# Kernel tuning notes

Measured on AMD Instinct MI355X. Metric: run time of the kernel, lower is better.

Reference implementation:

```python
import jax, jax.numpy as jnp
import numpy as np

N_NODES, N_EDGES, IN_FEATS, N_HIDDEN, K_HOP = 100000, 400000, 128, 128, 3


def setup_inputs() -> dict:
    key = jax.random.key(0)
    ks = jax.random.split(key, 12)
    x = jax.random.normal(ks[0], (N_NODES, IN_FEATS), jnp.float32)
    src = jax.random.randint(ks[1], (N_EDGES,), 0, N_NODES, jnp.int32)
    dst = jax.random.randint(ks[2], (N_EDGES,), 0, N_NODES, jnp.int32)
    neg_src = jax.random.randint(ks[3], (N_EDGES,), 0, N_NODES, jnp.int32)
    neg_dst = jax.random.randint(ks[4], (N_EDGES,), 0, N_NODES, jnp.int32)

    def lin(k, fan_in, fan_out):
        return jax.random.normal(k, (fan_in, fan_out), jnp.float32) / np.sqrt(fan_in).astype(np.float32)

    W_sg = lin(ks[5], IN_FEATS, N_HIDDEN)
    b_sg = jnp.zeros((N_HIDDEN,), jnp.float32)
    W1 = lin(ks[6], N_HIDDEN, N_HIDDEN)
    b1 = jnp.zeros((N_HIDDEN,), jnp.float32)
    W2 = lin(ks[7], N_HIDDEN, N_HIDDEN)
    b2 = jnp.zeros((N_HIDDEN,), jnp.float32)
    W3 = lin(ks[8], N_HIDDEN, 1)
    b3 = jnp.zeros((1,), jnp.float32)
    return {"x": x, "src": src, "dst": dst, "neg_src": neg_src, "neg_dst": neg_dst,
            "W_sg": W_sg, "b_sg": b_sg, "W1": W1, "b1": b1, "W2": W2, "b2": b2,
            "W3": W3, "b3": b3}


def reference(x, src, dst, neg_src, neg_dst, W_sg, b_sg, W1, b1, W2, b2, W3, b3):
    n = x.shape[0]
    # dgl.add_self_loop: append (i -> i) for every node
    loops = jnp.arange(n, dtype=src.dtype)
    s_all = jnp.concatenate([src, loops])
    d_all = jnp.concatenate([dst, loops])
    # SGConv 'both' norm: D^{-1/2} A D^{-1/2}, degrees = in-degrees (>=1 due to self loops)
    deg = jax.ops.segment_sum(jnp.ones_like(d_all, jnp.float32), d_all, num_segments=n)
    norm = jax.lax.rsqrt(jnp.maximum(deg, 1.0))[:, None]  # [N,1]
    h = x
    for _ in range(K_HOP):
        msg = (h * norm)[s_all]                                  # gather scaled source feats
        h = norm * jax.ops.segment_sum(msg, d_all, num_segments=n)
    h = h @ W_sg + b_sg  # SGConv final linear -> [N, n_hidden]

    def predict(h_s, h_d):
        z = h_s * h_d
        z = jax.nn.relu(z @ W1 + b1)
        z = jax.nn.relu(z @ W2 + b2)
        return z @ W3 + b3  # [E, 1]

    h_pos = predict(h[src], h[dst])
    h_neg = predict(h[neg_src], h[neg_dst])
    return (h_pos, h_neg)
```

## Files before the change

### kernel.cpp

```cpp
#include <hip/hip_runtime.h>

#define NN 100000
#define NE 400000
#define FD 128
#define SCAN_B 1024

typedef __attribute__((ext_vector_type(8))) short bf16x8;
typedef __attribute__((ext_vector_type(4))) float f32x4;

__device__ inline unsigned short f2bf(float f) {
    unsigned u = __float_as_uint(f);
    unsigned r = u + 0x7fff + ((u >> 16) & 1);
    return (unsigned short)(r >> 16);
}
__device__ inline unsigned mulbf2(unsigned a, unsigned c) {
    float a0 = __uint_as_float(a << 16), a1 = __uint_as_float(a & 0xffff0000u);
    float c0 = __uint_as_float(c << 16), c1 = __uint_as_float(c & 0xffff0000u);
    unsigned r0 = f2bf(a0 * c0);
    unsigned r1 = f2bf(a1 * c1);
    return r0 | (r1 << 16);
}
__device__ inline int zi(int row, int col) {
    return row * 128 + (((col >> 3) ^ (row & 7)) << 3) + (col & 7);
}

__global__ void k_deg_count(const int* __restrict__ key, int* __restrict__ deg) {
    int e = blockIdx.x * 256 + threadIdx.x;
    if (e < NE) atomicAdd(&deg[key[e]], 1);
}
__global__ void k_norm(const int* __restrict__ deg, float* __restrict__ norm) {
    int i = blockIdx.x * 256 + threadIdx.x;
    if (i < NN) norm[i] = rsqrtf((float)(deg[i] + 1));
}
__global__ __launch_bounds__(SCAN_B) void k_scan1(const int* __restrict__ deg,
                                                  int* __restrict__ off,
                                                  int* __restrict__ bsum) {
    __shared__ int s[SCAN_B];
    int t = threadIdx.x, g = blockIdx.x * SCAN_B + t;
    s[t] = (g < NN) ? deg[g] : 0;
    __syncthreads();
    for (int d = 1; d < SCAN_B; d <<= 1) {
        int add = (t >= d) ? s[t - d] : 0;
        __syncthreads();
        s[t] += add;
        __syncthreads();
    }
    if (g < NN) off[g + 1] = s[t];
    if (t == SCAN_B - 1) bsum[blockIdx.x] = s[t];
}
__global__ void k_scan2(int* __restrict__ bsum, int nb) {
    if (threadIdx.x == 0 && blockIdx.x == 0) {
        int acc = 0;
        for (int i = 0; i < nb; i++) { int v = bsum[i]; bsum[i] = acc; acc += v; }
    }
}
__global__ void k_scan3(int* __restrict__ off, const int* __restrict__ bsum) {
    int g = blockIdx.x * 256 + threadIdx.x;
    if (g == 0) off[0] = 0;
    if (g < NN) off[g + 1] += bsum[g / SCAN_B];
}
__global__ void k_cur(const int* __restrict__ off, int* __restrict__ cur) {
    int g = blockIdx.x * 256 + threadIdx.x;
    if (g < NN) cur[g] = off[g];
}
__global__ void k_fill_pn(const int* __restrict__ src, const int* __restrict__ dst,
                          const float* __restrict__ norm, int* __restrict__ cur,
                          int* __restrict__ csr, float* __restrict__ csn) {
    int e = blockIdx.x * 256 + threadIdx.x;
    if (e < NE) {
        int s = src[e];
        int p = atomicAdd(&cur[dst[e]], 1);
        csr[p] = s;
        csn[p] = norm[s];
    }
}

__global__ __launch_bounds__(256) void k_prop0(const float* __restrict__ x,
        const int* __restrict__ off, const int* __restrict__ csr,
        const float* __restrict__ csn, const float* __restrict__ norm,
        unsigned short* __restrict__ G1) {
    int t = blockIdx.x * 256 + threadIdx.x;
    int v = t >> 5, lane = t & 31;
    float nv = norm[v];
    float4 a = ((const float4*)(x + (size_t)v * FD))[lane];
    float ax = nv * a.x, ay = nv * a.y, az = nv * a.z, aw = nv * a.w;
    int j = off[v], j1 = off[v + 1];
    for (; j + 3 < j1; j += 4) {
        int s0 = csr[j], s1 = csr[j + 1], s2 = csr[j + 2], s3 = csr[j + 3];
        float n0 = csn[j], n1 = csn[j + 1], n2 = csn[j + 2], n3 = csn[j + 3];
        float4 b0 = ((const float4*)(x + (size_t)s0 * FD))[lane];
        float4 b1 = ((const float4*)(x + (size_t)s1 * FD))[lane];
        float4 b2 = ((const float4*)(x + (size_t)s2 * FD))[lane];
        float4 b3 = ((const float4*)(x + (size_t)s3 * FD))[lane];
        ax += n0 * b0.x + n1 * b1.x + n2 * b2.x + n3 * b3.x;
        ay += n0 * b0.y + n1 * b1.y + n2 * b2.y + n3 * b3.y;
        az += n0 * b0.z + n1 * b1.z + n2 * b2.z + n3 * b3.z;
        aw += n0 * b0.w + n1 * b1.w + n2 * b2.w + n3 * b3.w;
    }
    for (; j < j1; j++) {
        int s0 = csr[j];
        float n0 = csn[j];
        float4 b0 = ((const float4*)(x + (size_t)s0 * FD))[lane];
        ax += n0 * b0.x; ay += n0 * b0.y; az += n0 * b0.z; aw += n0 * b0.w;
    }
    float sc = nv * nv;
    unsigned lo = f2bf(sc * ax) | ((unsigned)f2bf(sc * ay) << 16);
    unsigned hi = f2bf(sc * az) | ((unsigned)f2bf(sc * aw) << 16);
    ((uint2*)(G1 + (size_t)v * FD))[lane] = make_uint2(lo, hi);
}

template <bool LAST>
__global__ __launch_bounds__(256) void k_prop(const unsigned short* __restrict__ Gin,
        const int* __restrict__ off, const int* __restrict__ csr,
        const float* __restrict__ norm, unsigned short* __restrict__ Gout) {
    int t = blockIdx.x * 256 + threadIdx.x;
    int v = t >> 5, lane = t & 31;
    float nv = norm[v];
    uint2 g = ((const uint2*)(Gin + (size_t)v * FD))[lane];
    float ax = __uint_as_float(g.x << 16), ay = __uint_as_float(g.x & 0xffff0000u);
    float az = __uint_as_float(g.y << 16), aw = __uint_as_float(g.y & 0xffff0000u);
    int j = off[v], j1 = off[v + 1];
    for (; j + 3 < j1; j += 4) {
        int s0 = csr[j], s1 = csr[j + 1], s2 = csr[j + 2], s3 = csr[j + 3];
        uint2 b0 = ((const uint2*)(Gin + (size_t)s0 * FD))[lane];
        uint2 b1 = ((const uint2*)(Gin + (size_t)s1 * FD))[lane];
        uint2 b2 = ((const uint2*)(Gin + (size_t)s2 * FD))[lane];
        uint2 b3 = ((const uint2*)(Gin + (size_t)s3 * FD))[lane];
        ax += __uint_as_float(b0.x << 16) + __uint_as_float(b1.x << 16)
            + __uint_as_float(b2.x << 16) + __uint_as_float(b3.x << 16);
        ay += __uint_as_float(b0.x & 0xffff0000u) + __uint_as_float(b1.x & 0xffff0000u)
            + __uint_as_float(b2.x & 0xffff0000u) + __uint_as_float(b3.x & 0xffff0000u);
        az += __uint_as_float(b0.y << 16) + __uint_as_float(b1.y << 16)
            + __uint_as_float(b2.y << 16) + __uint_as_float(b3.y << 16);
        aw += __uint_as_float(b0.y & 0xffff0000u) + __uint_as_float(b1.y & 0xffff0000u)
            + __uint_as_float(b2.y & 0xffff0000u) + __uint_as_float(b3.y & 0xffff0000u);
    }
    for (; j < j1; j++) {
        int s0 = csr[j];
        uint2 b0 = ((const uint2*)(Gin + (size_t)s0 * FD))[lane];
        ax += __uint_as_float(b0.x << 16);
        ay += __uint_as_float(b0.x & 0xffff0000u);
        az += __uint_as_float(b0.y << 16);
        aw += __uint_as_float(b0.y & 0xffff0000u);
    }
    float sc = LAST ? nv : nv * nv;
    unsigned lo = f2bf(sc * ax) | ((unsigned)f2bf(sc * ay) << 16);
    unsigned hi = f2bf(sc * az) | ((unsigned)f2bf(sc * aw) << 16);
    ((uint2*)(Gout + (size_t)v * FD))[lane] = make_uint2(lo, hi);
}

__global__ void k_pack_w(const float* __restrict__ Wsg, const float* __restrict__ W1,
                         const float* __restrict__ W2, uint4* __restrict__ wp) {
    int t = blockIdx.x * 256 + threadIdx.x;
    int wsel = t >> 11, r = t & 2047;
    const float* W = wsel == 0 ? Wsg : (wsel == 1 ? W1 : W2);
    int frag = r >> 6, l = r & 63;
    int nt = frag >> 2, kb = frag & 3;
    int col = 16 * nt + (l & 15);
    int k0 = 32 * kb + 8 * (l >> 4);
    unsigned q[4];
#pragma unroll
    for (int j = 0; j < 4; j++) {
        unsigned lo = f2bf(W[(size_t)(k0 + 2 * j) * FD + col]);
        unsigned hi = f2bf(W[(size_t)(k0 + 2 * j + 1) * FD + col]);
        q[j] = lo | (hi << 16);
    }
    wp[t] = make_uint4(q[0], q[1], q[2], q[3]);
}

__global__ __launch_bounds__(256, 4) void k_sgconv_mfma(const unsigned short* __restrict__ hin,
        const uint4* __restrict__ wp, const float* __restrict__ bsg,
        unsigned short* __restrict__ hout) {
    __shared__ unsigned short z[128 * 128];
    int tid = threadIdx.x;
    int row0 = blockIdx.x * 128;
#pragma unroll
    for (int it = 0; it < 8; it++) {
        int idx = it * 256 + tid;
        int r = idx >> 4, c = idx & 15;
        uint4 v = make_uint4(0, 0, 0, 0);
        if (row0 + r < NN) v = *(const uint4*)(hin + (size_t)(row0 + r) * FD + c * 8);
        *(uint4*)&z[zi(r, c * 8)] = v;
    }
    __syncthreads();

    int l = tid & 63, w = tid >> 6;
    f32x4 acc[2][8];
#pragma unroll
    for (int mt = 0; mt < 2; mt++)
#pragma unroll
        for (int nt = 0; nt < 8; nt++) acc[mt][nt] = (f32x4){0, 0, 0, 0};

#pragma unroll
    for (int kb = 0; kb < 4; kb++) {
        bf16x8 af[2];
#pragma unroll
        for (int mt = 0; mt < 2; mt++)
            af[mt] = *(const bf16x8*)&z[zi(w * 32 + mt * 16 + (l & 15), kb * 32 + (l >> 4) * 8)];
#pragma unroll
        for (int nt = 0; nt < 8; nt++) {
            bf16x8 wf = *(const bf16x8*)&wp[(nt * 4 + kb) * 64 + l];
#pragma unroll
            for (int mt = 0; mt < 2; mt++)
                acc[mt][nt] = __builtin_amdgcn_mfma_f32_16x16x32_bf16(af[mt], wf, acc[mt][nt], 0, 0, 0);
        }
    }
#pragma unroll
    for (int mt = 0; mt < 2; mt++)
#pragma unroll
        for (int nt = 0; nt < 8; nt++) {
            float bv = bsg[16 * nt + (l & 15)];
#pragma unroll
            for (int r = 0; r < 4; r++)
                z[zi(w * 32 + mt * 16 + (l >> 4) * 4 + r, 16 * nt + (l & 15))] =
                    f2bf(acc[mt][nt][r] + bv);
        }
    __syncthreads();
#pragma unroll
    for (int it = 0; it < 8; it++) {
        int idx = it * 256 + tid;
        int r = idx >> 4, c = idx & 15;
        if (row0 + r < NN)
            *(uint4*)(hout + (size_t)(row0 + r) * FD + c * 8) = *(const uint4*)&z[zi(r, c * 8)];
    }
}

#define ZS 136

__global__ __launch_bounds__(256, 4) void k_predict_mfma(const unsigned short* __restrict__ h,
        const int* __restrict__ srcA, const int* __restrict__ dstA,
        const int* __restrict__ srcB, const int* __restrict__ dstB,
        const uint4* __restrict__ w1p, const uint4* __restrict__ w2p,
        const float* __restrict__ b1, const float* __restrict__ b2,
        const float* __restrict__ W3, const float* __restrict__ b3,
        float* __restrict__ out) {
    __shared__ unsigned short z[128 * ZS];
    int tid = threadIdx.x;
    int b = blockIdx.x;
    int half = b >= 3125;
    int eb = (b - (half ? 3125 : 0)) * 128;
    const int* S = half ? srcB : srcA;
    const int* D = half ? dstB : dstA;
    int outbase = half ? NE : 0;

#pragma unroll
    for (int it = 0; it < 2; it++) {
        int e = (tid >> 2) + 64 * it;
        int p = tid & 3;
        int s = S[eb + e], d = D[eb + e];
        const uint4* hs = (const uint4*)(h + (size_t)s * FD + p * 32);
        const uint4* hd = (const uint4*)(h + (size_t)d * FD + p * 32);
        unsigned short* zr = z + e * ZS + p * 32;
#pragma unroll
        for (int q = 0; q < 4; q++) {
            uint4 a = hs[q], c = hd[q];
            uint4 r;
            r.x = mulbf2(a.x, c.x);
            r.y = mulbf2(a.y, c.y);
            r.z = mulbf2(a.z, c.z);
            r.w = mulbf2(a.w, c.w);
            *(uint4*)(zr + q * 8) = r;
        }
    }
    __syncthreads();

    int l = tid & 63, w = tid >> 6;
    f32x4 acc[2][8];
#pragma unroll
    for (int mt = 0; mt < 2; mt++)
#pragma unroll
        for (int nt = 0; nt < 8; nt++) acc[mt][nt] = (f32x4){0, 0, 0, 0};

#pragma unroll
    for (int kb = 0; kb < 4; kb++) {
        bf16x8 af[2];
#pragma unroll
        for (int mt = 0; mt < 2; mt++)
            af[mt] = *(const bf16x8*)&z[(w * 32 + mt * 16 + (l & 15)) * ZS + kb * 32 + (l >> 4) * 8];
#pragma unroll
        for (int nt = 0; nt < 8; nt++) {
            bf16x8 wf = *(const bf16x8*)&w1p[(nt * 4 + kb) * 64 + l];
#pragma unroll
            for (int mt = 0; mt < 2; mt++)
                acc[mt][nt] = __builtin_amdgcn_mfma_f32_16x16x32_bf16(af[mt], wf, acc[mt][nt], 0, 0, 0);
        }
    }
    __syncthreads();
#pragma unroll
    for (int mt = 0; mt < 2; mt++)
#pragma unroll
        for (int nt = 0; nt < 8; nt++) {
            float bv = b1[16 * nt + (l & 15)];
#pragma unroll
            for (int r = 0; r < 4; r++)
                z[(w * 32 + mt * 16 + (l >> 4) * 4 + r) * ZS + 16 * nt + (l & 15)] =
                    f2bf(fmaxf(acc[mt][nt][r] + bv, 0.0f));
        }
    __syncthreads();

#pragma unroll
    for (int mt = 0; mt < 2; mt++)
#pragma unroll
        for (int nt = 0; nt < 8; nt++) acc[mt][nt] = (f32x4){0, 0, 0, 0};
#pragma unroll
    for (int kb = 0; kb < 4; kb++) {
        bf16x8 af[2];
#pragma unroll
        for (int mt = 0; mt < 2; mt++)
            af[mt] = *(const bf16x8*)&z[(w * 32 + mt * 16 + (l & 15)) * ZS + kb * 32 + (l >> 4) * 8];
#pragma unroll
        for (int nt = 0; nt < 8; nt++) {
            bf16x8 wf = *(const bf16x8*)&w2p[(nt * 4 + kb) * 64 + l];
#pragma unroll
            for (int mt = 0; mt < 2; mt++)
                acc[mt][nt] = __builtin_amdgcn_mfma_f32_16x16x32_bf16(af[mt], wf, acc[mt][nt], 0, 0, 0);
        }
    }

    {
        float bb3 = b3[0];
#pragma unroll
        for (int mt = 0; mt < 2; mt++)
#pragma unroll
            for (int r = 0; r < 4; r++) {
                float p = 0.0f;
#pragma unroll
                for (int nt = 0; nt < 8; nt++)
                    p += fmaxf(acc[mt][nt][r] + b2[16 * nt + (l & 15)], 0.0f) * W3[16 * nt + (l & 15)];
                p += __shfl_xor(p, 1);
                p += __shfl_xor(p, 2);
                p += __shfl_xor(p, 4);
                p += __shfl_xor(p, 8);
                if ((l & 15) == 0)
                    out[outbase + eb + w * 32 + mt * 16 + (l >> 4) * 4 + r] = p + bb3;
            }
    }
}

extern "C" void kernel_launch(void* const* d_in, const int* in_sizes, int n_in,
                              void* d_out, int out_size, void* d_ws, size_t ws_size,
                              hipStream_t stream) {
    const float* x    = (const float*)d_in[0];
    const int* src    = (const int*)d_in[1];
    const int* dst    = (const int*)d_in[2];
    const int* nsrc   = (const int*)d_in[3];
    const int* ndst   = (const int*)d_in[4];
    const float* W_sg = (const float*)d_in[5];
    const float* b_sg = (const float*)d_in[6];
    const float* W1   = (const float*)d_in[7];
    const float* b1   = (const float*)d_in[8];
    const float* W2   = (const float*)d_in[9];
    const float* b2   = (const float*)d_in[10];
    const float* W3   = (const float*)d_in[11];
    const float* b3   = (const float*)d_in[12];
    float* out = (float*)d_out;

    char* p = (char*)d_ws;
    float* norm = (float*)p;  p += 400000;
    int*   deg  = (int*)p;    p += 400000;
    int*   off  = (int*)p;    p += 400128;
    int*   cur  = (int*)p;    p += 400000;
    int*   bsum = (int*)p;    p += 512;
    int*   csr  = (int*)p;    p += 1600000;
    float* csn  = (float*)p;  p += 1600000;
    uint4* wp   = (uint4*)p;  p += 98304;
    unsigned short* G1 = (unsigned short*)p;  p += (size_t)NN * FD * 2;
    unsigned short* G2 = (unsigned short*)p;
    unsigned short* h  = G1;
    unsigned short* hbf = G2;

    const int gN = (NN + 255) / 256;
    const int gE = (NE + 255) / 256;
    const int nb = (NN + SCAN_B - 1) / SCAN_B;

    k_pack_w<<<24, 256, 0, stream>>>(W_sg, W1, W2, wp);

    hipMemsetAsync(deg, 0, 400000, stream);
    k_deg_count<<<gE, 256, 0, stream>>>(dst, deg);
    k_norm<<<gN, 256, 0, stream>>>(deg, norm);
    k_scan1<<<nb, SCAN_B, 0, stream>>>(deg, off, bsum);
    k_scan2<<<1, 64, 0, stream>>>(bsum, nb);
    k_scan3<<<gN, 256, 0, stream>>>(off, bsum);
    k_cur<<<gN, 256, 0, stream>>>(off, cur);
    k_fill_pn<<<gE, 256, 0, stream>>>(src, dst, norm, cur, csr, csn);

    const int gP = NN * 32 / 256;
    k_prop0<<<gP, 256, 0, stream>>>(x, off, csr, csn, norm, G1);
    k_prop<false><<<gP, 256, 0, stream>>>(G1, off, csr, norm, G2);
    k_prop<true><<<gP, 256, 0, stream>>>(G2, off, csr, norm, h);

    k_sgconv_mfma<<<(NN + 127) / 128, 256, 0, stream>>>(h, wp, b_sg, hbf);

    k_predict_mfma<<<6250, 256, 0, stream>>>(hbf, src, dst, nsrc, ndst,
                                             wp + 2048, wp + 4096,
                                             b1, b2, W3, b3, out);
}
```

Baseline: 291.4 us.

## Prescale features to bf16, reuse generic prop for first hop, fuse setup kernels

Adds a kernel that scales x by norm and converts it to bf16, so the first propagation hop reuses the bf16 k_prop kernel instead of an fp32 gather kernel with per-edge norm values. The per-edge csn array goes away. k_norm is merged into scan1 and k_cur into scan3, and the serial block-sum scan becomes a wavefront shuffle scan. The first-hop gathers move half the bytes, at the cost of an extra full pass over x and earlier bf16 rounding of the input.

```diff
diff --git a/kernel.cpp b/kernel.cpp
--- a/kernel.cpp
+++ b/kernel.cpp
@@ -28,16 +28,15 @@
     int e = blockIdx.x * 256 + threadIdx.x;
     if (e < NE) atomicAdd(&deg[key[e]], 1);
 }
-__global__ void k_norm(const int* __restrict__ deg, float* __restrict__ norm) {
-    int i = blockIdx.x * 256 + threadIdx.x;
-    if (i < NN) norm[i] = rsqrtf((float)(deg[i] + 1));
-}
 __global__ __launch_bounds__(SCAN_B) void k_scan1(const int* __restrict__ deg,
                                                   int* __restrict__ off,
-                                                  int* __restrict__ bsum) {
+                                                  int* __restrict__ bsum,
+                                                  float* __restrict__ norm) {
     __shared__ int s[SCAN_B];
     int t = threadIdx.x, g = blockIdx.x * SCAN_B + t;
-    s[t] = (g < NN) ? deg[g] : 0;
+    int d0 = (g < NN) ? deg[g] : 0;
+    if (g < NN) norm[g] = rsqrtf((float)(d0 + 1));
+    s[t] = d0;
     __syncthreads();
     for (int d = 1; d < SCAN_B; d <<= 1) {
         int add = (t >= d) ? s[t - d] : 0;
@@ -49,64 +48,52 @@
     if (t == SCAN_B - 1) bsum[blockIdx.x] = s[t];
 }
 __global__ void k_scan2(int* __restrict__ bsum, int nb) {
-    if (threadIdx.x == 0 && blockIdx.x == 0) {
-        int acc = 0;
-        for (int i = 0; i < nb; i++) { int v = bsum[i]; bsum[i] = acc; acc += v; }
-    }
-}
-__global__ void k_scan3(int* __restrict__ off, const int* __restrict__ bsum) {
+    int l = threadIdx.x;
+    int v0 = (l < nb) ? bsum[l] : 0;
+    int v1 = (64 + l < nb) ? bsum[64 + l] : 0;
+    int a = v0;
+    for (int d = 1; d < 64; d <<= 1) {
+        int t = __shfl_up(a, d, 64);
+        if (l >= d) a += t;
+    }
+    int tot0 = __shfl(a, 63, 64);
+    int b = v1;
+    for (int d = 1; d < 64; d <<= 1) {
+        int t = __shfl_up(b, d, 64);
+        if (l >= d) b += t;
+    }
+    if (l < nb) bsum[l] = a - v0;
+    if (64 + l < nb) bsum[64 + l] = tot0 + b - v1;
+}
+__global__ void k_scan3(int* __restrict__ off, const int* __restrict__ bsum,
+                        int* __restrict__ cur) {
     int g = blockIdx.x * 256 + threadIdx.x;
-    if (g == 0) off[0] = 0;
-    if (g < NN) off[g + 1] += bsum[g / SCAN_B];
-}
-__global__ void k_cur(const int* __restrict__ off, int* __restrict__ cur) {
-    int g = blockIdx.x * 256 + threadIdx.x;
-    if (g < NN) cur[g] = off[g];
-}
-__global__ void k_fill_pn(const int* __restrict__ src, const int* __restrict__ dst,
-                          const float* __restrict__ norm, int* __restrict__ cur,
-                          int* __restrict__ csr, float* __restrict__ csn) {
+    if (g == 0) { off[0] = 0; cur[0] = 0; }
+    if (g < NN) {
+        int v = off[g + 1] + bsum[g / SCAN_B];
+        off[g + 1] = v;
+        cur[g + 1] = v;
+    }
+}
+__global__ void k_fill(const int* __restrict__ src, const int* __restrict__ dst,
+                       int* __restrict__ cur, int* __restrict__ csr) {
     int e = blockIdx.x * 256 + threadIdx.x;
     if (e < NE) {
-        int s = src[e];
         int p = atomicAdd(&cur[dst[e]], 1);
-        csr[p] = s;
-        csn[p] = norm[s];
-    }
-}
-
-__global__ __launch_bounds__(256) void k_prop0(const float* __restrict__ x,
-        const int* __restrict__ off, const int* __restrict__ csr,
-        const float* __restrict__ csn, const float* __restrict__ norm,
-        unsigned short* __restrict__ G1) {
-    int t = blockIdx.x * 256 + threadIdx.x;
-    int v = t >> 5, lane = t & 31;
+        csr[p] = src[e];
+    }
+}
+
+__global__ __launch_bounds__(256) void k_scale(const float* __restrict__ x,
+        const float* __restrict__ norm, unsigned short* __restrict__ xs) {
+    int i = blockIdx.x * 256 + threadIdx.x;
+    if (i >= NN * (FD / 4)) return;
+    int v = i >> 5;
     float nv = norm[v];
-    float4 a = ((const float4*)(x + (size_t)v * FD))[lane];
-    float ax = nv * a.x, ay = nv * a.y, az = nv * a.z, aw = nv * a.w;
-    int j = off[v], j1 = off[v + 1];
-    for (; j + 3 < j1; j += 4) {
-        int s0 = csr[j], s1 = csr[j + 1], s2 = csr[j + 2], s3 = csr[j + 3];
-        float n0 = csn[j], n1 = csn[j + 1], n2 = csn[j + 2], n3 = csn[j + 3];
-        float4 b0 = ((const float4*)(x + (size_t)s0 * FD))[lane];
-        float4 b1 = ((const float4*)(x + (size_t)s1 * FD))[lane];
-        float4 b2 = ((const float4*)(x + (size_t)s2 * FD))[lane];
-        float4 b3 = ((const float4*)(x + (size_t)s3 * FD))[lane];
-        ax += n0 * b0.x + n1 * b1.x + n2 * b2.x + n3 * b3.x;
-        ay += n0 * b0.y + n1 * b1.y + n2 * b2.y + n3 * b3.y;
-        az += n0 * b0.z + n1 * b1.z + n2 * b2.z + n3 * b3.z;
-        aw += n0 * b0.w + n1 * b1.w + n2 * b2.w + n3 * b3.w;
-    }
-    for (; j < j1; j++) {
-        int s0 = csr[j];
-        float n0 = csn[j];
-        float4 b0 = ((const float4*)(x + (size_t)s0 * FD))[lane];
-        ax += n0 * b0.x; ay += n0 * b0.y; az += n0 * b0.z; aw += n0 * b0.w;
-    }
-    float sc = nv * nv;
-    unsigned lo = f2bf(sc * ax) | ((unsigned)f2bf(sc * ay) << 16);
-    unsigned hi = f2bf(sc * az) | ((unsigned)f2bf(sc * aw) << 16);
-    ((uint2*)(G1 + (size_t)v * FD))[lane] = make_uint2(lo, hi);
+    float4 a = ((const float4*)x)[i];
+    unsigned lo = f2bf(nv * a.x) | ((unsigned)f2bf(nv * a.y) << 16);
+    unsigned hi = f2bf(nv * a.z) | ((unsigned)f2bf(nv * a.w) << 16);
+    ((uint2*)xs)[i] = make_uint2(lo, hi);
 }
 
 template <bool LAST>
@@ -359,11 +346,11 @@
     float* norm = (float*)p;  p += 400000;
     int*   deg  = (int*)p;    p += 400000;
     int*   off  = (int*)p;    p += 400128;
-    int*   cur  = (int*)p;    p += 400000;
+    int*   cur  = (int*)p;    p += 400128;
     int*   bsum = (int*)p;    p += 512;
     int*   csr  = (int*)p;    p += 1600000;
-    float* csn  = (float*)p;  p += 1600000;
     uint4* wp   = (uint4*)p;  p += 98304;
+    unsigned short* xs = (unsigned short*)p;  p += (size_t)NN * FD * 2;
     unsigned short* G1 = (unsigned short*)p;  p += (size_t)NN * FD * 2;
     unsigned short* G2 = (unsigned short*)p;
     unsigned short* h  = G1;
@@ -372,20 +359,20 @@
     const int gN = (NN + 255) / 256;
     const int gE = (NE + 255) / 256;
     const int nb = (NN + SCAN_B - 1) / SCAN_B;
+    const int g4 = (NN * (FD / 4) + 255) / 256;
 
     k_pack_w<<<24, 256, 0, stream>>>(W_sg, W1, W2, wp);
 
     hipMemsetAsync(deg, 0, 400000, stream);
     k_deg_count<<<gE, 256, 0, stream>>>(dst, deg);
-    k_norm<<<gN, 256, 0, stream>>>(deg, norm);
-    k_scan1<<<nb, SCAN_B, 0, stream>>>(deg, off, bsum);
+    k_scan1<<<nb, SCAN_B, 0, stream>>>(deg, off, bsum, norm);
     k_scan2<<<1, 64, 0, stream>>>(bsum, nb);
-    k_scan3<<<gN, 256, 0, stream>>>(off, bsum);
-    k_cur<<<gN, 256, 0, stream>>>(off, cur);
-    k_fill_pn<<<gE, 256, 0, stream>>>(src, dst, norm, cur, csr, csn);
-
+    k_scan3<<<gN, 256, 0, stream>>>(off, bsum, cur);
+    k_fill<<<gE, 256, 0, stream>>>(src, dst, cur, csr);
+
+    k_scale<<<g4, 256, 0, stream>>>(x, norm, xs);
     const int gP = NN * 32 / 256;
-    k_prop0<<<gP, 256, 0, stream>>>(x, off, csr, csn, norm, G1);
+    k_prop<false><<<gP, 256, 0, stream>>>(xs, off, csr, norm, G1);
     k_prop<false><<<gP, 256, 0, stream>>>(G1, off, csr, norm, G2);
     k_prop<true><<<gP, 256, 0, stream>>>(G2, off, csr, norm, h);
 
```

Result: faster. 278.6 us (median of 2 runs) (-4.4%).
